# Kernel tuning notes

Hardware: AMD Instinct MI355X
Metric: run time of the kernel (lower is better)

Reference implementation:

```python
import jax, jax.numpy as jnp
import numpy as np

QMAX = 127.0  # 2**(bits-1) - 1 for bits=8, signed symmetric


def _quantize_signed_symmetric(t):
    # per-tensor symmetric: scale = max|t| / qmax, q = clamp(round(t/scale))
    scale = jnp.max(jnp.abs(t)) / QMAX
    q = jnp.clip(jnp.round(t / scale), -QMAX, QMAX)
    return q, scale


def setup_inputs() -> dict:
    key = jax.random.key(0)
    k1, k2, k3 = jax.random.split(key, 3)
    N, D_IN, D_OUT = 16384, 1024, 1024
    x = jax.random.normal(k1, (N, D_IN), dtype=jnp.float32)
    weight = jax.random.normal(k2, (D_OUT, D_IN), dtype=jnp.float32) * 0.02
    bias = jax.random.normal(k3, (D_OUT,), dtype=jnp.float32) * 0.01
    return {"x": x, "weight": weight, "bias": bias}


def reference(x, weight, bias):
    # weight quantization (cached in torch; recomputed here, same math)
    qw, w_scale = _quantize_signed_symmetric(weight)
    qw_t = qw.astype(jnp.int32).T            # [D_IN, D_OUT]
    # activation quantization
    qx, x_scale = _quantize_signed_symmetric(x)
    qx = qx.astype(jnp.int32)                # [N, D_IN]
    # int32 matmul, then per-tensor dequant + bias
    acc = qx @ qw_t                          # int32 [N, D_OUT]
    y = acc.astype(jnp.float32) * (x_scale * w_scale)
    return y + bias
```

## Files before the change

### kernel.cpp

```cpp
#include <hip/hip_runtime.h>

#define QMAX 127.0f

typedef int int4v __attribute__((ext_vector_type(4)));
typedef float float4v __attribute__((ext_vector_type(4)));

__device__ __forceinline__ float amax4(float4 v) {
    return fmaxf(fmaxf(fabsf(v.x), fabsf(v.y)), fmaxf(fabsf(v.z), fabsf(v.w)));
}

__global__ void absmax2_kernel(const float4* __restrict__ px, int n4x,
                               const float4* __restrict__ pw, int n4w,
                               int gx, int* __restrict__ amax) {
    const float4* p; int n4; int* out; int nb, bid;
    if ((int)blockIdx.x < gx) { p = px; n4 = n4x; out = amax + 0; nb = gx; bid = blockIdx.x; }
    else { p = pw; n4 = n4w; out = amax + 1; nb = gridDim.x - gx; bid = blockIdx.x - gx; }
    const int S = nb * blockDim.x;
    int i = bid * blockDim.x + threadIdx.x;
    float a = 0.f, b = 0.f, c = 0.f, d = 0.f;
    for (; i + 3 * S < n4; i += 4 * S) {
        float4 v0 = p[i];
        float4 v1 = p[i + S];
        float4 v2 = p[i + 2 * S];
        float4 v3 = p[i + 3 * S];
        a = fmaxf(a, amax4(v0));
        b = fmaxf(b, amax4(v1));
        c = fmaxf(c, amax4(v2));
        d = fmaxf(d, amax4(v3));
    }
    for (; i < n4; i += S) a = fmaxf(a, amax4(p[i]));
    float m = fmaxf(fmaxf(a, b), fmaxf(c, d));
    for (int off = 32; off; off >>= 1) m = fmaxf(m, __shfl_down(m, off, 64));
    __shared__ float sm[4];
    if ((threadIdx.x & 63) == 0) sm[threadIdx.x >> 6] = m;
    __syncthreads();
    if (threadIdx.x == 0) {
        float bm = fmaxf(fmaxf(sm[0], sm[1]), fmaxf(sm[2], sm[3]));
        atomicMax(out, (int)__float_as_uint(bm));
    }
}

__device__ __forceinline__ int qone(float v, float s) {
    float q = fminf(fmaxf(rintf(v / s), -QMAX), QMAX);
    return (int)q;
}
__device__ __forceinline__ int qpack4(float4 v, float s) {
    return (qone(v.x, s) & 255) | ((qone(v.y, s) & 255) << 8) |
           ((qone(v.z, s) & 255) << 16) | ((qone(v.w, s) & 255) << 24);
}

__global__ void quantw_kernel(const float4* __restrict__ sw, int4v* __restrict__ dw,
                              int n16w, int kshift, int KC,
                              const int* __restrict__ amax) {
    const float scale = __uint_as_float((unsigned)amax[1]) / QMAX;
    const int stride = gridDim.x * blockDim.x;
    for (int i = blockIdx.x * blockDim.x + threadIdx.x; i < n16w; i += stride) {
        float4 v0 = sw[4 * i + 0];
        float4 v1 = sw[4 * i + 1];
        float4 v2 = sw[4 * i + 2];
        float4 v3 = sw[4 * i + 3];
        int4v o = { qpack4(v0, scale), qpack4(v1, scale),
                    qpack4(v2, scale), qpack4(v3, scale) };
        const int n = i >> kshift;
        const int kg = i & ((1 << kshift) - 1);
        const int kc = kg >> 2, q = kg & 3;
        const int g = n >> 4, r = n & 15;
        dw[(g * KC + kc) * 64 + q * 16 + r] = o;
    }
}

__global__ __launch_bounds__(512, 2) void gemm_i8_kernel(
        const float* __restrict__ x, const char* __restrict__ qb,
        const float4* __restrict__ bias4, const int* __restrict__ amax,
        float* __restrict__ out, int M, int N, int K) {
    extern __shared__ char sA[];

    const int KC = K >> 6;
    const int tid = threadIdx.x;
    const int lane = tid & 63;
    const int w = tid >> 6;
    const int m0 = blockIdx.x * 64;

    const float xs = __uint_as_float((unsigned)amax[0]) / QMAX;
    int4v* sAv_w = (int4v*)sA;
    const int kcs = __builtin_ctz(KC);
    const int PPW = KC >> 1;
#pragma unroll 2
    for (int p = 0; p < PPW; ++p) {
        const int pair = w * PPW + p;
        const int i = pair >> kcs;
        const int kc = pair & (KC - 1);
        const int row = m0 + i * 16 + (lane & 15);
        const int k0 = kc * 64 + (lane >> 4) * 16;
        const float4* src = (const float4*)(x + (size_t)row * K + k0);
        float4 v0 = src[0];
        float4 v1 = src[1];
        float4 v2 = src[2];
        float4 v3 = src[3];
        int4v o = { qpack4(v0, xs), qpack4(v1, xs),
                    qpack4(v2, xs), qpack4(v3, xs) };
        sAv_w[i * K + kc * 64 + lane] = o;
    }
    __syncthreads();

    int4v acc[8][4];
    const int4v zero = {0, 0, 0, 0};
#pragma unroll
    for (int j = 0; j < 8; ++j)
#pragma unroll
        for (int i = 0; i < 4; ++i) acc[j][i] = zero;

    const int4v* sAv = (const int4v*)sA;
    const char* bbase = qb + (size_t)(w * 8) * KC * 1024 + lane * 16;

#define LOADB(Bb, kc)                                                        \
    do { _Pragma("unroll") for (int j = 0; j < 8; ++j)                       \
        Bb[j] = *(const int4v*)(bbase + ((size_t)j * KC + (kc)) * 1024);     \
    } while (0)
#define LOADA(Af, kc)                                                        \
    do { _Pragma("unroll") for (int i = 0; i < 4; ++i)                       \
        Af[i] = sAv[i * K + (kc) * 64 + lane];                               \
    } while (0)
#define MF(Bb, Af)                                                           \
    do { _Pragma("unroll") for (int j = 0; j < 8; ++j)                       \
        _Pragma("unroll") for (int i = 0; i < 4; ++i)                        \
            acc[j][i] = __builtin_amdgcn_mfma_i32_16x16x64_i8(               \
                Bb[j], Af[i], acc[j][i], 0, 0, 0);                           \
    } while (0)

    int4v B0[8], B1[8], Af[4];
    LOADB(B0, 0);
#pragma unroll 1
    for (int kc = 0; kc + 2 < KC; kc += 2) {
        LOADB(B1, kc + 1);
        LOADA(Af, kc);
        MF(B0, Af);
        LOADB(B0, kc + 2);
        LOADA(Af, kc + 1);
        MF(B1, Af);
    }
    LOADB(B1, KC - 1);
    LOADA(Af, KC - 2);
    MF(B0, Af);
    LOADA(Af, KC - 1);
    MF(B1, Af);

    const float sc = (__uint_as_float((unsigned)amax[0]) / QMAX) *
                     (__uint_as_float((unsigned)amax[1]) / QMAX);
    const int quad = lane >> 4;
    const int rbase = m0 + (lane & 15);
    const int cb4 = w * 32;
#pragma unroll
    for (int j = 0; j < 8; ++j) {
        const float4 bv = bias4[cb4 + j * 4 + quad];
#pragma unroll
        for (int i = 0; i < 4; ++i) {
            const int row = rbase + i * 16;
            float4v v;
            v[0] = (float)acc[j][i][0] * sc + bv.x;
            v[1] = (float)acc[j][i][1] * sc + bv.y;
            v[2] = (float)acc[j][i][2] * sc + bv.z;
            v[3] = (float)acc[j][i][3] * sc + bv.w;
            *((float4v*)(out + (size_t)row * N) + cb4 + j * 4 + quad) = v;
        }
    }
}

extern "C" void kernel_launch(void* const* d_in, const int* in_sizes, int n_in,
                              void* d_out, int out_size, void* d_ws, size_t ws_size,
                              hipStream_t stream) {
    const float* x = (const float*)d_in[0];
    const float* w = (const float*)d_in[1];
    const float* bias = (const float*)d_in[2];
    float* out = (float*)d_out;

    const int xn = in_sizes[0];
    const int wn = in_sizes[1];
    const int N = in_sizes[2];
    const int K = wn / N;
    const int M = xn / K;
    const int KC = K >> 6;
    const int kshift = __builtin_ctz(K >> 4);

    int* amax = (int*)d_ws;
    char* qw = (char*)d_ws + 1024;

    const int GAX = 2048, GAW = 256;
    absmax2_kernel<<<GAX + GAW, 256, 0, stream>>>(
        (const float4*)x, xn / 4, (const float4*)w, wn / 4, GAX, amax);

    quantw_kernel<<<256, 256, 0, stream>>>(
        (const float4*)w, (int4v*)qw, wn / 16, kshift, KC, amax);

    gemm_i8_kernel<<<M / 64, 512, 64 * K, stream>>>(
        x, qw, (const float4*)bias, amax, out, M, N, K);
}
```

Measured before the change: 166.4 us.

## Halve GEMM row tile to 32 and raise occupancy to four blocks per CU

Cuts the per-block M tile from 64 to 32 rows, so LDS per block and accumulator registers are halved, and launch bounds now allow four blocks per CU. The B-fragment pipeline is restructured to double-buffer half-sets of four fragments per k-step, with the first B load issued before the activation quantization. Each block now rereads the full quantized weight from global/L2 for half as many rows, doubling weight traffic in exchange for more resident waves to hide latency.

```diff
diff --git a/kernel.cpp b/kernel.cpp
--- a/kernel.cpp
+++ b/kernel.cpp
@@ -69,7 +69,7 @@
     }
 }
 
-__global__ __launch_bounds__(512, 2) void gemm_i8_kernel(
+__global__ __launch_bounds__(512, 4) void gemm_i8_kernel(
         const float* __restrict__ x, const char* __restrict__ qb,
         const float4* __restrict__ bias4, const int* __restrict__ amax,
         float* __restrict__ out, int M, int N, int K) {
@@ -79,12 +79,33 @@
     const int tid = threadIdx.x;
     const int lane = tid & 63;
     const int w = tid >> 6;
-    const int m0 = blockIdx.x * 64;
+    const int m0 = blockIdx.x * 32;
+
+    const char* bbase = qb + (size_t)(w * 8) * KC * 1024 + lane * 16;
+
+#define LOADB4(Bb, kc, h)                                                    \
+    do { _Pragma("unroll") for (int j = 0; j < 4; ++j)                       \
+        Bb[j] = *(const int4v*)(bbase +                                      \
+                 (((size_t)((h) * 4 + j)) * KC + (kc)) * 1024);              \
+    } while (0)
+#define LOADA(Af, kc)                                                        \
+    do { _Pragma("unroll") for (int i = 0; i < 2; ++i)                       \
+        Af[i] = sAv[i * K + (kc) * 64 + lane];                               \
+    } while (0)
+#define MFH(Bb, Af, h)                                                       \
+    do { _Pragma("unroll") for (int j = 0; j < 4; ++j)                       \
+        _Pragma("unroll") for (int i = 0; i < 2; ++i)                        \
+            acc[(h) * 4 + j][i] = __builtin_amdgcn_mfma_i32_16x16x64_i8(     \
+                Bb[j], Af[i], acc[(h) * 4 + j][i], 0, 0, 0);                 \
+    } while (0)
+
+    int4v B0[4], B1[4], Af[2];
+    LOADB4(B0, 0, 0);
 
     const float xs = __uint_as_float((unsigned)amax[0]) / QMAX;
     int4v* sAv_w = (int4v*)sA;
     const int kcs = __builtin_ctz(KC);
-    const int PPW = KC >> 1;
+    const int PPW = KC >> 2;
 #pragma unroll 2
     for (int p = 0; p < PPW; ++p) {
         const int pair = w * PPW + p;
@@ -103,47 +124,27 @@
     }
     __syncthreads();
 
-    int4v acc[8][4];
+    int4v acc[8][2];
     const int4v zero = {0, 0, 0, 0};
 #pragma unroll
     for (int j = 0; j < 8; ++j)
 #pragma unroll
-        for (int i = 0; i < 4; ++i) acc[j][i] = zero;
+        for (int i = 0; i < 2; ++i) acc[j][i] = zero;
 
     const int4v* sAv = (const int4v*)sA;
-    const char* bbase = qb + (size_t)(w * 8) * KC * 1024 + lane * 16;
 
-#define LOADB(Bb, kc)                                                        \
-    do { _Pragma("unroll") for (int j = 0; j < 8; ++j)                       \
-        Bb[j] = *(const int4v*)(bbase + ((size_t)j * KC + (kc)) * 1024);     \
-    } while (0)
-#define LOADA(Af, kc)                                                        \
-    do { _Pragma("unroll") for (int i = 0; i < 4; ++i)                       \
-        Af[i] = sAv[i * K + (kc) * 64 + lane];                               \
-    } while (0)
-#define MF(Bb, Af)                                                           \
-    do { _Pragma("unroll") for (int j = 0; j < 8; ++j)                       \
-        _Pragma("unroll") for (int i = 0; i < 4; ++i)                        \
-            acc[j][i] = __builtin_amdgcn_mfma_i32_16x16x64_i8(               \
-                Bb[j], Af[i], acc[j][i], 0, 0, 0);                           \
-    } while (0)
-
-    int4v B0[8], B1[8], Af[4];
-    LOADB(B0, 0);
 #pragma unroll 1
-    for (int kc = 0; kc + 2 < KC; kc += 2) {
-        LOADB(B1, kc + 1);
+    for (int kc = 0; kc < KC - 1; ++kc) {
+        LOADB4(B1, kc, 1);
         LOADA(Af, kc);
-        MF(B0, Af);
-        LOADB(B0, kc + 2);
-        LOADA(Af, kc + 1);
-        MF(B1, Af);
+        MFH(B0, Af, 0);
+        LOADB4(B0, kc + 1, 0);
+        MFH(B1, Af, 1);
     }
-    LOADB(B1, KC - 1);
-    LOADA(Af, KC - 2);
-    MF(B0, Af);
+    LOADB4(B1, KC - 1, 1);
     LOADA(Af, KC - 1);
-    MF(B1, Af);
+    MFH(B0, Af, 0);
+    MFH(B1, Af, 1);
 
     const float sc = (__uint_as_float((unsigned)amax[0]) / QMAX) *
                      (__uint_as_float((unsigned)amax[1]) / QMAX);
@@ -154,7 +155,7 @@
     for (int j = 0; j < 8; ++j) {
         const float4 bv = bias4[cb4 + j * 4 + quad];
 #pragma unroll
-        for (int i = 0; i < 4; ++i) {
+        for (int i = 0; i < 2; ++i) {
             const int row = rbase + i * 16;
             float4v v;
             v[0] = (float)acc[j][i][0] * sc + bv.x;
@@ -192,6 +193,6 @@
     quantw_kernel<<<256, 256, 0, stream>>>(
         (const float4*)w, (int4v*)qw, wn / 16, kshift, KC, amax);
 
-    gemm_i8_kernel<<<M / 64, 512, 64 * K, stream>>>(
+    gemm_i8_kernel<<<M / 32, 512, 32 * K, stream>>>(
         x, qw, (const float4*)bias, amax, out, M, N, K);
 }
```

New measurement: 170.4 us. +2.4%, slower.
